# Kernel tuning notes

Hardware: AMD Instinct MI355X
Metric: run time of the kernel (lower is better)

## Reference

```python
import jax, jax.numpy as jnp
import numpy as np

D2, D1, T1, T2, D3, T3 = 120, 40, 10, 5, 3, 1


def _kaiming_uniform(key, shape):
    # torch kaiming_uniform_ with nonlinearity='relu': bound = sqrt(6/fan_in), fan_in = shape[1]
    bound = np.sqrt(6.0 / shape[1])
    return jax.random.uniform(key, shape, jnp.float32, -bound, bound)


def setup_inputs() -> dict:
    key = jax.random.key(0)
    ks = jax.random.split(key, 6)
    x = jax.random.normal(ks[0], (131072, D1, T1), jnp.float32)
    return {
        "x": x,
        "BL_W1": _kaiming_uniform(ks[1], (D2, D1)),
        "BL_W2": _kaiming_uniform(ks[2], (T1, T2)),
        "BL_B": jnp.zeros((D2, T2), jnp.float32),
        "T_W1": _kaiming_uniform(ks[3], (D3, D2)),
        "T_W": jnp.full((T2, T2), 1.0 / T2, jnp.float32),
        "T_W2": _kaiming_uniform(ks[4], (T2, T3)),
        "T_B": jnp.zeros((D3, T3), jnp.float32),
        "l": jnp.full((1,), 0.5, jnp.float32),
    }


def _max_norm(w):
    # torch max_norm_: if frobenius norm > 10, rescale to norm 10 (done under no_grad)
    n = jnp.linalg.norm(w)
    scale = jnp.where(n > 10.0, 10.0 / (1e-8 + n), 1.0)
    return w * jax.lax.stop_gradient(scale)


def reference(x, BL_W1, BL_W2, BL_B, T_W1, T_W, T_W2, T_B, l):
    # --- weight clamps performed at the top of m_btabl.forward ---
    W1a = _max_norm(BL_W1)
    W2a = _max_norm(BL_W2)
    W1b = _max_norm(T_W1)
    Wb = _max_norm(T_W)
    W2b = _max_norm(T_W2)
    lam = jnp.clip(l[0], 0.0, 1.0)  # l.data clamped to [0,1]

    # BL layer: relu(W1 @ x @ W2 + B); x: [B, D1, T1] -> [B, D2, T2]
    h = jax.nn.relu(jnp.einsum('ed,bdt->bet', W1a, x) @ W2a + BL_B)
    # dropout(0.1) is identity at inference

    # TABL layer (t1 here = T2 = 5)
    X = jnp.einsum('ed,bdt->bet', W1b, h)          # [B, D3, T2]
    eye = jnp.eye(T2, dtype=jnp.float32)
    Wm = Wb - Wb * eye + eye / T2                  # force diagonal to 1/t1
    A = jax.nn.softmax(X @ Wm, axis=-1)            # temporal attention
    X = lam * X + (1.0 - lam) * X * A              # convex combination
    y = X @ W2b + T_B                              # [B, D3, 1]

    y = jnp.squeeze(y)                             # [B, D3]
    return jax.nn.softmax(y, axis=1)
```

## Files before the change

kernel.cpp:

```cpp
#include <hip/hip_runtime.h>


typedef short bf16x8 __attribute__((ext_vector_type(8)));
typedef float f32x4v __attribute__((ext_vector_type(4)));

#define NTP 256
#define NTM 320

__device__ __forceinline__ unsigned short f2bf(float f) {
    unsigned int u = __float_as_uint(f);
    u += 0x7FFFu + ((u >> 16) & 1u);
    return (unsigned short)(u >> 16);
}

__device__ __forceinline__ float block_reduce_sum(float v, float* red, int tid) {
    #pragma unroll
    for (int off = 32; off > 0; off >>= 1) v += __shfl_xor(v, off, 64);
    if ((tid & 63) == 0) red[tid >> 6] = v;
    __syncthreads();
    float r = red[0] + red[1] + red[2] + red[3];
    __syncthreads();
    return r;
}

__global__ __launch_bounds__(NTP)
void prep_kernel(const float* __restrict__ W1, const float* __restrict__ W2,
                 const float* __restrict__ B,  const float* __restrict__ Tw1,
                 const float* __restrict__ Tw, const float* __restrict__ Tw2,
                 const float* __restrict__ TB, const float* __restrict__ l,
                 float* __restrict__ ws)
{
    __shared__ float red[4];
    const int tid = threadIdx.x;
    float ss;
    ss = 0.f; for (int i = tid; i < 4800; i += NTP) { float w = W1[i];  ss += w*w; }
    const float n1 = sqrtf(block_reduce_sum(ss, red, tid));
    ss = 0.f; for (int i = tid; i < 50;   i += NTP) { float w = W2[i];  ss += w*w; }
    const float n2 = sqrtf(block_reduce_sum(ss, red, tid));
    ss = 0.f; for (int i = tid; i < 360;  i += NTP) { float w = Tw1[i]; ss += w*w; }
    const float n3 = sqrtf(block_reduce_sum(ss, red, tid));
    ss = 0.f; for (int i = tid; i < 25;   i += NTP) { float w = Tw[i];  ss += w*w; }
    const float n4 = sqrtf(block_reduce_sum(ss, red, tid));
    ss = 0.f; for (int i = tid; i < 5;    i += NTP) { float w = Tw2[i]; ss += w*w; }
    const float n5 = sqrtf(block_reduce_sum(ss, red, tid));

    const float s1 = n1 > 10.f ? 10.f/(1e-8f+n1) : 1.f;
    const float s2 = n2 > 10.f ? 10.f/(1e-8f+n2) : 1.f;
    const float s3 = n3 > 10.f ? 10.f/(1e-8f+n3) : 1.f;
    const float s4 = n4 > 10.f ? 10.f/(1e-8f+n4) : 1.f;
    const float s5 = n5 > 10.f ? 10.f/(1e-8f+n5) : 1.f;

    unsigned short* img = (unsigned short*)ws;
    for (int i = tid; i < 129*48; i += NTP) {
        const int e = i / 48, k = i - e*48;
        float v = 0.f;
        if (e < 120) {
            if (k < 40)      v = W1[e*40 + k] * s1;
            else if (k < 45) v = B[e*5 + (k-40)];
        }
        img[i] = f2bf(v);
    }
    for (int i = tid; i < 512; i += NTP) {
        const int e = i >> 2, c = i & 3;
        ws[3096 + i] = (c < 3 && e < 120) ? Tw1[c*120 + e] * s3 : 0.f;
    }
    for (int i = tid; i < 36; i += NTP) {
        float v = 0.f;
        if (i < 25)      { int r = i/5, c = i - r*5; v = (r == c) ? 0.2f : Tw[i]*s4; }
        else if (i < 30) v = Tw2[i-25] * s5;
        else if (i < 33) v = TB[i-30];
        else if (i == 33){ float lv = l[0]; v = fminf(fmaxf(lv, 0.f), 1.f); }
        ws[3608 + i] = v;
    }
    for (int i = tid; i < 50; i += NTP) ws[3644 + i] = W2[i] * s2;
}

__global__ __launch_bounds__(NTM)
void btabl_main(const float* __restrict__ x, const float* __restrict__ ws,
                float* __restrict__ out, int nsamp)
{
    __align__(16) __shared__ unsigned short sW1[129*48];
    __align__(16) __shared__ float          sWp[128*4];
    __align__(16) __shared__ float          sC[36];
    __align__(16) __shared__ unsigned short sZ[320*48 + 16];
    __align__(16) __shared__ float          sX3[320*3];

    const int tid = threadIdx.x;

    {
        const float4* src = (const float4*)ws;
        float4* d1 = (float4*)sW1;
        for (int i = tid; i < 774; i += NTM) d1[i] = src[i];
        float4* d2 = (float4*)sWp;
        for (int i = tid; i < 128; i += NTM) d2[i] = src[774 + i];
        if (tid < 9) ((float4*)sC)[tid] = src[902 + tid];
    }

    {
        const int sLoc = tid / 5, c = tid - sLoc*5;
        const int sGlob = blockIdx.x * 64 + sLoc;
        const int sClamp = sGlob < nsamp ? sGlob : (nsamp - 1);
        const float* W2p = ws + 3644;
        const float* xs = x + (size_t)sClamp*400 + c*80;

        float Zf[8][5];
        #pragma unroll
        for (int hh = 0; hh < 2; hh++) {
            const float4* xv = (const float4*)(xs + hh*40);
            float xf[40];
            #pragma unroll
            for (int i = 0; i < 10; i++) {
                float4 q = xv[i];
                xf[i*4+0] = q.x; xf[i*4+1] = q.y; xf[i*4+2] = q.z; xf[i*4+3] = q.w;
            }
            #pragma unroll
            for (int r = 0; r < 4; r++) {
                #pragma unroll
                for (int t = 0; t < 5; t++) {
                    float a = 0.f;
                    #pragma unroll
                    for (int k = 0; k < 10; k++)
                        a = fmaf(xf[r*10+k], W2p[k*5+t], a);
                    Zf[hh*4+r][t] = a;
                }
            }
        }
        const int colBase = 5 * sLoc;
        #pragma unroll
        for (int t = 0; t < 5; t++) {
            bf16x8 zv;
            #pragma unroll
            for (int r = 0; r < 8; r++) zv[r] = (short)f2bf(Zf[r][t]);
            *(bf16x8*)(sZ + (colBase + t)*48 + c*8) = zv;
        }
        bf16x8 oh = {0,0,0,0,0,0,0,0};
        oh[c] = (short)0x3F80;
        *(bf16x8*)(sZ + (colBase + c)*48 + 40) = oh;
    }
    __syncthreads();

    const int wave = tid >> 6;
    const int lane = tid & 63;
    const int quad = lane >> 4;
    const int m    = lane & 15;
    const int colBase = wave * 64;

    bf16x8 Bf[4][2];
    const bf16x8 z8 = {0,0,0,0,0,0,0,0};
    #pragma unroll
    for (int nt = 0; nt < 4; nt++) {
        const int col = colBase + nt*16 + m;
        Bf[nt][0] = *(const bf16x8*)(sZ + col*48 + quad*8);
        bf16x8 b1 = *(const bf16x8*)(sZ + col*48 + 32 + quad*8);
        Bf[nt][1] = (quad >= 2) ? z8 : b1;
    }

    float X3p[4][3];
    #pragma unroll
    for (int nt = 0; nt < 4; nt++)
        #pragma unroll
        for (int j = 0; j < 3; j++) X3p[nt][j] = 0.f;

    const f32x4v zacc = {0.f, 0.f, 0.f, 0.f};
    #pragma unroll
    for (int mt = 0; mt < 8; mt++) {
        const unsigned short* arow = sW1 + (mt*16 + m)*48;
        const bf16x8 A0 = *(const bf16x8*)(arow + quad*8);
        const bf16x8 A1 = *(const bf16x8*)(arow + 32 + quad*8);
        f32x4v wp[4];
        #pragma unroll
        for (int r = 0; r < 4; r++)
            wp[r] = *(const f32x4v*)(sWp + (mt*16 + quad*4 + r)*4);
        #pragma unroll
        for (int nt = 0; nt < 4; nt++) {
            f32x4v acc = __builtin_amdgcn_mfma_f32_16x16x32_bf16(A0, Bf[nt][0], zacc, 0, 0, 0);
            acc = __builtin_amdgcn_mfma_f32_16x16x32_bf16(A1, Bf[nt][1], acc, 0, 0, 0);
            #pragma unroll
            for (int r = 0; r < 4; r++) {
                const float h = fmaxf(acc[r], 0.f);
                X3p[nt][0] = fmaf(wp[r][0], h, X3p[nt][0]);
                X3p[nt][1] = fmaf(wp[r][1], h, X3p[nt][1]);
                X3p[nt][2] = fmaf(wp[r][2], h, X3p[nt][2]);
            }
        }
    }

    #pragma unroll
    for (int nt = 0; nt < 4; nt++) {
        #pragma unroll
        for (int j = 0; j < 3; j++) {
            float v = X3p[nt][j];
            v += __shfl_xor(v, 16, 64);
            v += __shfl_xor(v, 32, 64);
            X3p[nt][j] = v;
        }
    }
    if (quad == 0) {
        #pragma unroll
        for (int nt = 0; nt < 4; nt++) {
            const int col = colBase + nt*16 + m;
            sX3[col*3 + 0] = X3p[nt][0];
            sX3[col*3 + 1] = X3p[nt][1];
            sX3[col*3 + 2] = X3p[nt][2];
        }
    }
    __syncthreads();

    if (tid < 64) {
        const int sGlob = blockIdx.x * 64 + tid;
        float X3v[3][5];
        #pragma unroll
        for (int t = 0; t < 5; t++)
            #pragma unroll
            for (int j = 0; j < 3; j++)
                X3v[j][t] = sX3[(tid*5 + t)*3 + j];

        const float lam  = sC[33];
        const float olam = 1.f - lam;
        float y[3];
        #pragma unroll
        for (int j = 0; j < 3; j++) {
            float S[5];
            #pragma unroll
            for (int t = 0; t < 5; t++) {
                float a = 0.f;
                #pragma unroll
                for (int k = 0; k < 5; k++)
                    a = fmaf(X3v[j][k], sC[k*5 + t], a);
                S[t] = a;
            }
            float mx = S[0];
            #pragma unroll
            for (int t = 1; t < 5; t++) mx = fmaxf(mx, S[t]);
            float ex[5], se = 0.f;
            #pragma unroll
            for (int t = 0; t < 5; t++) { ex[t] = __expf(S[t] - mx); se += ex[t]; }
            const float inv = 1.f / se;
            float yj = sC[30 + j];
            #pragma unroll
            for (int t = 0; t < 5; t++) {
                const float a  = ex[t] * inv;
                const float xc = X3v[j][t] * (lam + olam * a);
                yj = fmaf(xc, sC[25 + t], yj);
            }
            y[j] = yj;
        }
        const float mx = fmaxf(y[0], fmaxf(y[1], y[2]));
        const float e0 = __expf(y[0]-mx), e1 = __expf(y[1]-mx), e2 = __expf(y[2]-mx);
        const float inv = 1.f / (e0 + e1 + e2);
        if (sGlob < nsamp) {
            float* o = out + (size_t)sGlob*3;
            o[0] = e0*inv; o[1] = e1*inv; o[2] = e2*inv;
        }
    }
}

extern "C" void kernel_launch(void* const* d_in, const int* in_sizes, int n_in,
                              void* d_out, int out_size, void* d_ws, size_t ws_size,
                              hipStream_t stream) {
    const float* x   = (const float*)d_in[0];
    const float* W1  = (const float*)d_in[1];
    const float* W2  = (const float*)d_in[2];
    const float* B   = (const float*)d_in[3];
    const float* Tw1 = (const float*)d_in[4];
    const float* Tw  = (const float*)d_in[5];
    const float* Tw2 = (const float*)d_in[6];
    const float* TB  = (const float*)d_in[7];
    const float* l   = (const float*)d_in[8];
    float* out = (float*)d_out;
    float* ws  = (float*)d_ws;

    hipLaunchKernelGGL(prep_kernel, dim3(1), dim3(NTP), 0, stream,
                       W1, W2, B, Tw1, Tw, Tw2, TB, l, ws);

    const int nsamp = in_sizes[0] / 400;
    const int grid  = (nsamp + 63) / 64;
    hipLaunchKernelGGL(btabl_main, dim3(grid), dim3(NTM), 0, stream,
                       x, ws, out, nsamp);
}
```

Measured before the change: 381.1 us.

## Stage x through LDS with async double-buffered global_load_lds pipeline

Replaces the per-thread direct global loads of x, where each thread read an 80-float strided slice, with a double-buffered pipeline. Chunks of 8 samples are staged into LDS using global_load_lds, manual vmcnt waits and barriers. Each thread then computes one d-row of the W2 product from LDS, with W2 cached in registers, and writes bf16 results into sZ. The aim is coalesced loads and overlap of memory latency with compute. In exchange it adds 25KB of LDS plus many barriers and limits occupancy to one block per SIMD via launch bounds.

Result: faster. 359.0 us (-5.8%).

```diff
diff --git a/kernel.cpp b/kernel.cpp
--- a/kernel.cpp
+++ b/kernel.cpp
@@ -1,4 +1,5 @@
 #include <hip/hip_runtime.h>
+#include <stdint.h>
 
 
 typedef short bf16x8 __attribute__((ext_vector_type(8)));
@@ -6,6 +7,8 @@
 
 #define NTP 256
 #define NTM 320
+#define GAS __attribute__((address_space(1)))
+#define LAS __attribute__((address_space(3)))
 
 __device__ __forceinline__ unsigned short f2bf(float f) {
     unsigned int u = __float_as_uint(f);
@@ -75,72 +78,108 @@
     for (int i = tid; i < 50; i += NTP) ws[3644 + i] = W2[i] * s2;
 }
 
-__global__ __launch_bounds__(NTM)
+
+__device__ __forceinline__ void stage_chunk(const char* xB, size_t base, size_t gmax,
+                                            float* lbuf, int wave, int lane)
+{
+    #pragma unroll
+    for (int i = 0; i < 3; i++) {
+        if (i < 2 || lane < 32) {
+            const int unit = wave*160 + i*64 + lane;
+            size_t go = base + (size_t)unit*16;
+            if (go > gmax) go = gmax;
+            __builtin_amdgcn_global_load_lds(
+                (const GAS unsigned int*)(xB + go),
+                (LAS unsigned int*)(lbuf + (wave*160 + i*64)*4),
+                16, 0, 0);
+        }
+    }
+}
+
+__global__ __launch_bounds__(NTM, 1)
 void btabl_main(const float* __restrict__ x, const float* __restrict__ ws,
                 float* __restrict__ out, int nsamp)
 {
     __align__(16) __shared__ unsigned short sW1[129*48];
     __align__(16) __shared__ float          sWp[128*4];
     __align__(16) __shared__ float          sC[36];
+    __align__(16) __shared__ float          sW2[52];
     __align__(16) __shared__ unsigned short sZ[320*48 + 16];
     __align__(16) __shared__ float          sX3[320*3];
-
-    const int tid = threadIdx.x;
+    __align__(16) __shared__ float          xb[2][3200];
+
+    const int tid  = threadIdx.x;
+    const int wave = tid >> 6;
+    const int lane = tid & 63;
 
     {
         const float4* src = (const float4*)ws;
         float4* d1 = (float4*)sW1;
-        for (int i = tid; i < 774; i += NTM) d1[i] = src[i];
-        float4* d2 = (float4*)sWp;
-        for (int i = tid; i < 128; i += NTM) d2[i] = src[774 + i];
-        if (tid < 9) ((float4*)sC)[tid] = src[902 + tid];
+        #pragma unroll
+        for (int i = 0; i < 3; i++) {
+            const int idx = tid + i*NTM;
+            if (idx < 774) d1[idx] = src[idx];
+        }
+        if (tid < 128) ((float4*)sWp)[tid] = src[774 + tid];
+        if (tid < 9)   ((float4*)sC)[tid]  = src[902 + tid];
+        if (tid < 12)  ((float4*)sW2)[tid] = src[911 + tid];
+        if (tid < 2)   sW2[48 + tid] = ws[3692 + tid];
     }
 
     {
-        const int sLoc = tid / 5, c = tid - sLoc*5;
-        const int sGlob = blockIdx.x * 64 + sLoc;
-        const int sClamp = sGlob < nsamp ? sGlob : (nsamp - 1);
-        const float* W2p = ws + 3644;
-        const float* xs = x + (size_t)sClamp*400 + c*80;
-
-        float Zf[8][5];
-        #pragma unroll
-        for (int hh = 0; hh < 2; hh++) {
-            const float4* xv = (const float4*)(xs + hh*40);
-            float xf[40];
-            #pragma unroll
-            for (int i = 0; i < 10; i++) {
-                float4 q = xv[i];
-                xf[i*4+0] = q.x; xf[i*4+1] = q.y; xf[i*4+2] = q.z; xf[i*4+3] = q.w;
-            }
-            #pragma unroll
-            for (int r = 0; r < 4; r++) {
-                #pragma unroll
-                for (int t = 0; t < 5; t++) {
-                    float a = 0.f;
-                    #pragma unroll
-                    for (int k = 0; k < 10; k++)
-                        a = fmaf(xf[r*10+k], W2p[k*5+t], a);
-                    Zf[hh*4+r][t] = a;
-                }
-            }
-        }
-        const int colBase = 5 * sLoc;
+        bf16x8 oh = {0,0,0,0,0,0,0,0};
+        oh[tid % 5] = (short)0x3F80;
+        *(bf16x8*)(sZ + tid*48 + 40) = oh;
+    }
+
+    __syncthreads();
+
+    const int sC8 = tid / 40;
+    const int dR  = tid - sC8*40;
+    const char*  xB        = (const char*)x;
+    const size_t blockBase = (size_t)blockIdx.x * 102400;
+    const size_t gmax      = (size_t)nsamp * 1600 - 16;
+
+    stage_chunk(xB, blockBase,          gmax, xb[0], wave, lane);
+    stage_chunk(xB, blockBase + 12800,  gmax, xb[1], wave, lane);
+
+    float W2r[50];
+    #pragma unroll
+    for (int i = 0; i < 50; i++) W2r[i] = sW2[i];
+
+    #pragma unroll
+    for (int r = 0; r < 8; r++) {
+        float* xbuf = xb[r & 1];
+        if (r < 7) { asm volatile("s_waitcnt vmcnt(3)" ::: "memory"); }
+        else       { asm volatile("s_waitcnt vmcnt(0)" ::: "memory"); }
+        asm volatile("s_barrier" ::: "memory");
+
+        const float* xr = xbuf + sC8*400 + dR*10;
+        float xf[10];
+        #pragma unroll
+        for (int q = 0; q < 5; q++) {
+            const float2 v = *(const float2*)(xr + q*2);
+            xf[2*q] = v.x; xf[2*q+1] = v.y;
+        }
+        float z[5];
         #pragma unroll
         for (int t = 0; t < 5; t++) {
-            bf16x8 zv;
-            #pragma unroll
-            for (int r = 0; r < 8; r++) zv[r] = (short)f2bf(Zf[r][t]);
-            *(bf16x8*)(sZ + (colBase + t)*48 + c*8) = zv;
-        }
-        bf16x8 oh = {0,0,0,0,0,0,0,0};
-        oh[c] = (short)0x3F80;
-        *(bf16x8*)(sZ + (colBase + c)*48 + 40) = oh;
-    }
-    __syncthreads();
-
-    const int wave = tid >> 6;
-    const int lane = tid & 63;
+            float a = 0.f;
+            #pragma unroll
+            for (int k = 0; k < 10; k++) a = fmaf(xf[k], W2r[k*5+t], a);
+            z[t] = a;
+        }
+        const int colB = (r*8 + sC8)*5;
+        unsigned short* zp = sZ + colB*48 + dR;
+        #pragma unroll
+        for (int t = 0; t < 5; t++) zp[t*48] = f2bf(z[t]);
+
+        asm volatile("s_barrier" ::: "memory");
+        if (r < 6)
+            stage_chunk(xB, blockBase + (size_t)(r+2)*12800, gmax, xb[r & 1], wave, lane);
+    }
+    __syncthreads();
+
     const int quad = lane >> 4;
     const int m    = lane & 15;
     const int colBase = wave * 64;
```

## Remap x loading so consecutive threads read contiguous rows and add occupancy hint

Applied to the files above, without the earlier changes.

The first stage now has each thread handle 20 contiguous floats (two rows) of a sample across four sample groups. Previously each thread read 80 floats of one sample. This makes neighbouring threads read adjacent memory, improving global-load coalescing, and lowers per-thread register pressure by dropping the 8x5 accumulator array. The one-hot rows are written in a separate pass with an extra barrier, LDS writes become 32-bit packed stores, and launch_bounds now requests 4 blocks per CU, which could force register spilling.

Result: faster. 334.2 us (-12.3%).

```diff
diff --git a/kernel.cpp b/kernel.cpp
--- a/kernel.cpp
+++ b/kernel.cpp
@@ -1,4 +1,5 @@
 #include <hip/hip_runtime.h>
+#include <stdint.h>
 
 
 typedef short bf16x8 __attribute__((ext_vector_type(8)));
@@ -75,7 +76,7 @@
     for (int i = tid; i < 50; i += NTP) ws[3644 + i] = W2[i] * s2;
 }
 
-__global__ __launch_bounds__(NTM)
+__global__ __launch_bounds__(NTM, 4)
 void btabl_main(const float* __restrict__ x, const float* __restrict__ ws,
                 float* __restrict__ out, int nsamp)
 {
@@ -85,62 +86,64 @@
     __align__(16) __shared__ unsigned short sZ[320*48 + 16];
     __align__(16) __shared__ float          sX3[320*3];
 
-    const int tid = threadIdx.x;
+    const int tid  = threadIdx.x;
+    const int wave = tid >> 6;
+    const int lane = tid & 63;
 
     {
         const float4* src = (const float4*)ws;
         float4* d1 = (float4*)sW1;
-        for (int i = tid; i < 774; i += NTM) d1[i] = src[i];
-        float4* d2 = (float4*)sWp;
-        for (int i = tid; i < 128; i += NTM) d2[i] = src[774 + i];
-        if (tid < 9) ((float4*)sC)[tid] = src[902 + tid];
+        #pragma unroll
+        for (int i = 0; i < 3; i++) {
+            const int idx = tid + i*NTM;
+            if (idx < 774) d1[idx] = src[idx];
+        }
+        if (tid < 128) ((float4*)sWp)[tid] = src[774 + tid];
+        if (tid < 9)   ((float4*)sC)[tid]  = src[902 + tid];
     }
 
     {
-        const int sLoc = tid / 5, c = tid - sLoc*5;
-        const int sGlob = blockIdx.x * 64 + sLoc;
-        const int sClamp = sGlob < nsamp ? sGlob : (nsamp - 1);
+        bf16x8 oh = {0,0,0,0,0,0,0,0};
+        oh[tid % 5] = (short)0x3F80;
+        *(bf16x8*)(sZ + tid*48 + 40) = oh;
+    }
+    __syncthreads();
+
+    {
+        const int p   = tid;
+        const int s16 = p / 20;
+        const int r20 = p - s16*20;
         const float* W2p = ws + 3644;
-        const float* xs = x + (size_t)sClamp*400 + c*80;
-
-        float Zf[8][5];
-        #pragma unroll
-        for (int hh = 0; hh < 2; hh++) {
-            const float4* xv = (const float4*)(xs + hh*40);
-            float xf[40];
-            #pragma unroll
-            for (int i = 0; i < 10; i++) {
-                float4 q = xv[i];
+
+        #pragma unroll
+        for (int r = 0; r < 4; r++) {
+            int sG = blockIdx.x*64 + r*16 + s16;
+            sG = sG < nsamp ? sG : (nsamp - 1);
+            const float4* xv = (const float4*)(x + (size_t)sG*400 + r20*20);
+            float xf[20];
+            #pragma unroll
+            for (int i = 0; i < 5; i++) {
+                const float4 q = xv[i];
                 xf[i*4+0] = q.x; xf[i*4+1] = q.y; xf[i*4+2] = q.z; xf[i*4+3] = q.w;
             }
-            #pragma unroll
-            for (int r = 0; r < 4; r++) {
+            const int col0 = (r*16 + s16)*5;
+            #pragma unroll
+            for (int t = 0; t < 5; t++) {
+                float z0 = 0.f, z1 = 0.f;
                 #pragma unroll
-                for (int t = 0; t < 5; t++) {
-                    float a = 0.f;
-                    #pragma unroll
-                    for (int k = 0; k < 10; k++)
-                        a = fmaf(xf[r*10+k], W2p[k*5+t], a);
-                    Zf[hh*4+r][t] = a;
+                for (int k = 0; k < 10; k++) {
+                    const float w = W2p[k*5 + t];
+                    z0 = fmaf(xf[k],      w, z0);
+                    z1 = fmaf(xf[10 + k], w, z1);
                 }
-            }
-        }
-        const int colBase = 5 * sLoc;
-        #pragma unroll
-        for (int t = 0; t < 5; t++) {
-            bf16x8 zv;
-            #pragma unroll
-            for (int r = 0; r < 8; r++) zv[r] = (short)f2bf(Zf[r][t]);
-            *(bf16x8*)(sZ + (colBase + t)*48 + c*8) = zv;
-        }
-        bf16x8 oh = {0,0,0,0,0,0,0,0};
-        oh[c] = (short)0x3F80;
-        *(bf16x8*)(sZ + (colBase + c)*48 + 40) = oh;
-    }
-    __syncthreads();
-
-    const int wave = tid >> 6;
-    const int lane = tid & 63;
+                const unsigned int pk =
+                    (unsigned int)f2bf(z0) | ((unsigned int)f2bf(z1) << 16);
+                *(unsigned int*)(sZ + (col0 + t)*48 + 2*r20) = pk;
+            }
+        }
+    }
+    __syncthreads();
+
     const int quad = lane >> 4;
     const int m    = lane & 15;
     const int colBase = wave * 64;
```
